# Kernel tuning notes

Hardware: AMD Instinct MI355X
Metric: run time of the kernel (lower is better)

Reference implementation:

```python
import jax, jax.numpy as jnp
import numpy as np

INPUT_SIZE = 64
HIDDEN = 128
BATCH = 512
SEQ = 512


def setup_inputs() -> dict:
    key = jax.random.key(0)
    ks = jax.random.split(key, 7)
    s_ih = 1.0 / np.sqrt(HIDDEN)
    token = jax.random.normal(ks[0], (BATCH, SEQ, INPUT_SIZE), dtype=jnp.float32)
    W_ih = jax.random.uniform(ks[1], (HIDDEN, INPUT_SIZE), jnp.float32, -s_ih, s_ih)
    W_hh = jax.random.uniform(ks[2], (HIDDEN, HIDDEN), jnp.float32, -s_ih, s_ih)
    b_ih = jax.random.uniform(ks[3], (HIDDEN,), jnp.float32, -s_ih, s_ih)
    b_hh = jax.random.uniform(ks[4], (HIDDEN,), jnp.float32, -s_ih, s_ih)
    W_lin = jax.random.uniform(ks[5], (1, HIDDEN), jnp.float32, -s_ih, s_ih)
    b_lin = jax.random.uniform(ks[6], (1,), jnp.float32, -s_ih, s_ih)
    return {"token": token, "W_ih": W_ih, "W_hh": W_hh, "b_ih": b_ih,
            "b_hh": b_hh, "W_lin": W_lin, "b_lin": b_lin}


def reference(token, W_ih, W_hh, b_ih, b_hh, W_lin, b_lin):
    # Precompute input projection for all timesteps: [T, B, H]
    x_proj = jnp.einsum('bti,hi->tbh', token, W_ih) + b_ih + b_hh
    h0 = jnp.zeros((token.shape[0], W_hh.shape[0]), dtype=token.dtype)

    def step(h, xp):
        h_new = jnp.tanh(xp + h @ W_hh.T)
        return h_new, None

    h_last, _ = jax.lax.scan(step, h0, x_proj)
    # Linear head on last hidden state: [B, 1]
    return h_last @ W_lin.T + b_lin
```

## Files before the change

### kernel.cpp

```cpp
#include <hip/hip_runtime.h>

#define B_ 512
#define T_ 512
#define I_ 64
#define H_ 128

#define HB0    0
#define HB1    512
#define DUMMY  1024
#define LDS_SZ 1280

#define FM(a, x, w) "v_fmac_f32 v" #a ", v" #x ", v" #w "\n\t"
#define SC(n) "v_mul_f32 v" #n ", 0x4038aa3b, v" #n "\n\t"

#define CLOBS \
    "v48","v49","v50","v51","v52","v53","v54","v55","v56","v57","v58","v59", \
    "v60","v61","v62","v63","v64","v65","v66","v67","v68","v69","v70","v71", \
    "v72","v73","v74","v75","v76","v77","v78","v79","v80","v81","v82","v83", \
    "v84","v85","v86","v87","v88","v89","v90","v91","v92","v93","v94","v95", \
    "v96","v97","v98","v99","v100","v101","v102","v103","v104","v105","v106", \
    "v107","v108","v109","v110","v111","v112","v113","v114","v115","v116", \
    "v117","v118","v119","v120","v121","v122","v123","v124","v125","v126", \
    "v127","memory"

#define RNN_STEP(TA, TB, TC, TD, HRD, HWR)                                    \
    asm volatile(                                                             \
        "ds_read_b128 v[72:75], %1\n\t"                                       \
        "ds_read_b128 v[76:79], %1 offset:256\n\t"                            \
        "s_waitcnt vmcnt(3)\n\t"                                              \
        "v_fma_f32 v48, v" #TA ", v112, %3\n\t"                               \
        "v_fma_f32 v49, v" #TA ", v116, %4\n\t"                               \
        "v_fma_f32 v50, v" #TA ", v120, %5\n\t"                               \
        "v_fma_f32 v51, v" #TA ", v124, %6\n\t"                               \
        FM(48,TB,113) FM(49,TB,117) FM(50,TB,121) FM(51,TB,125)               \
        FM(48,TC,114) FM(49,TC,118) FM(50,TC,122) FM(51,TC,126)               \
        FM(48,TD,115) FM(49,TD,119) FM(50,TD,123) FM(51,TD,127)               \
        "global_load_dwordx4 v[" #TA ":" #TD "], %0, %9\n\t"                  \
        "v_add_u32 %0, 0x100, %0\n\t"                                         \
        "v_and_b32 %0, 0x1ffff, %0\n\t"                                       \
        "s_waitcnt lgkmcnt(1)\n\t"                                            \
        FM(48,72,80) FM(49,72,88) FM(50,72,96)  FM(51,72,104)                 \
        FM(48,73,81) FM(49,73,89) FM(50,73,97)  FM(51,73,105)                 \
        FM(48,74,82) FM(49,74,90) FM(50,74,98)  FM(51,74,106)                 \
        FM(48,75,83) FM(49,75,91) FM(50,75,99)  FM(51,75,107)                 \
        "s_waitcnt lgkmcnt(0)\n\t"                                            \
        FM(48,76,84) FM(49,76,92) FM(50,76,100) FM(51,76,108)                 \
        FM(48,77,85) FM(49,77,93) FM(50,77,101) FM(51,77,109)                 \
        FM(48,78,86) FM(49,78,94) FM(50,78,102) FM(51,78,110)                 \
        FM(48,79,87) FM(49,79,95) FM(50,79,103) FM(51,79,111)                 \
        "s_nop 1\n\t"                                                         \
        "v_add_f32 v48, v48, v48 quad_perm:[1,0,3,2] row_mask:0xf bank_mask:0xf\n\t" \
        "v_add_f32 v49, v49, v49 quad_perm:[1,0,3,2] row_mask:0xf bank_mask:0xf\n\t" \
        "v_add_f32 v50, v50, v50 quad_perm:[1,0,3,2] row_mask:0xf bank_mask:0xf\n\t" \
        "v_add_f32 v51, v51, v51 quad_perm:[1,0,3,2] row_mask:0xf bank_mask:0xf\n\t" \
        "v_cndmask_b32 v52, v48, v49, %7\n\t"                                 \
        "v_cndmask_b32 v53, v50, v51, %7\n\t"                                 \
        "s_nop 0\n\t"                                                         \
        "v_add_f32 v52, v52, v52 quad_perm:[2,3,0,1] row_mask:0xf bank_mask:0xf\n\t" \
        "v_add_f32 v53, v53, v53 quad_perm:[2,3,0,1] row_mask:0xf bank_mask:0xf\n\t" \
        "v_cndmask_b32 v54, v52, v53, %8\n\t"                                 \
        "s_nop 1\n\t"                                                         \
        "v_add_f32 v54, v54, v54 row_shl:8 row_mask:0xf bank_mask:0x3\n\t"    \
        "s_nop 1\n\t"                                                         \
        "v_add_f32 v54, v54, v54 row_shl:4 row_mask:0xf bank_mask:0x1\n\t"    \
        "s_nop 1\n\t"                                                         \
        "v_exp_f32 v54, v54\n\t"                                              \
        "s_nop 0\n\t"                                                         \
        "v_add_f32 v54, 1.0, v54\n\t"                                         \
        "v_rcp_f32 v55, v54\n\t"                                              \
        "s_nop 0\n\t"                                                         \
        "v_fma_f32 v54, v55, -2.0, 1.0\n\t"                                   \
        "ds_write_b32 %2, v54\n\t"                                            \
        "s_waitcnt lgkmcnt(0)\n\t"                                            \
        "s_barrier"                                                           \
        : "+v"(voff)                                                          \
        : "v"(HRD), "v"(HWR), "v"(biasA), "v"(biasB), "v"(biasC),             \
          "v"(biasD), "s"(M1), "s"(M2), "s"(sbase)                            \
        : CLOBS)

__global__ __launch_bounds__(512) __attribute__((amdgpu_waves_per_eu(4, 4)))
void rnn_kernel(const float* __restrict__ token,
                const float* __restrict__ W_ih,
                const float* __restrict__ W_hh,
                const float* __restrict__ b_ih,
                const float* __restrict__ b_hh,
                const float* __restrict__ W_lin,
                const float* __restrict__ b_lin,
                float* __restrict__ out)
{
    __shared__ __align__(16) char lds[LDS_SZ];
    const unsigned lb =
        (unsigned)(uintptr_t)(__attribute__((address_space(3))) char*)lds;

    const int tid = threadIdx.x;
    const int e   = tid & 15;
    const int G   = tid >> 4;
    const int b   = blockIdx.x;
    const int jb  = 4 * G;

    {
        const float* pWh = W_hh + jb * H_ + e * 8;
        const float* pWi = W_ih + jb * I_ + e * 4;
        asm volatile(
            "global_load_dwordx4 v[80:83],   %0, off\n\t"
            "global_load_dwordx4 v[84:87],   %0, off offset:16\n\t"
            "global_load_dwordx4 v[88:91],   %0, off offset:512\n\t"
            "global_load_dwordx4 v[92:95],   %0, off offset:528\n\t"
            "global_load_dwordx4 v[96:99],   %0, off offset:1024\n\t"
            "global_load_dwordx4 v[100:103], %0, off offset:1040\n\t"
            "global_load_dwordx4 v[104:107], %0, off offset:1536\n\t"
            "global_load_dwordx4 v[108:111], %0, off offset:1552\n\t"
            "global_load_dwordx4 v[112:115], %1, off\n\t"
            "global_load_dwordx4 v[116:119], %1, off offset:256\n\t"
            "global_load_dwordx4 v[120:123], %1, off offset:512\n\t"
            "global_load_dwordx4 v[124:127], %1, off offset:768\n\t"
            "s_waitcnt vmcnt(0)\n\t"
            SC(80) SC(81) SC(82) SC(83) SC(84) SC(85) SC(86) SC(87)
            SC(88) SC(89) SC(90) SC(91) SC(92) SC(93) SC(94) SC(95)
            SC(96) SC(97) SC(98) SC(99) SC(100) SC(101) SC(102) SC(103)
            SC(104) SC(105) SC(106) SC(107) SC(108) SC(109) SC(110) SC(111)
            SC(112) SC(113) SC(114) SC(115) SC(116) SC(117) SC(118) SC(119)
            SC(120) SC(121) SC(122) SC(123) SC(124) SC(125) SC(126) SC(127)
            :: "v"(pWh), "v"(pWi) : CLOBS);
    }

    const float k16 = 2.885390081777927f / 16.0f;
    const float biasA = (b_ih[jb + 0] + b_hh[jb + 0]) * k16;
    const float biasB = (b_ih[jb + 1] + b_hh[jb + 1]) * k16;
    const float biasC = (b_ih[jb + 2] + b_hh[jb + 2]) * k16;
    const float biasD = (b_ih[jb + 3] + b_hh[jb + 3]) * k16;
    const unsigned long long M1 = 0xAAAAAAAAAAAAAAAAULL;
    const unsigned long long M2 = 0xCCCCCCCCCCCCCCCCULL;

    const int  jsel   = jb + (e & 3);
    const int  wbyte  = ((((jsel >> 2) & 1) * 16 + (jsel >> 3)) * 16) + (jsel & 3) * 4;
    const bool writer = (e < 4);
    const unsigned dmy = lb + DUMMY + (tid & 63) * 4;
    const unsigned hw0 = writer ? (lb + HB1 + wbyte) : dmy;
    const unsigned hw1 = writer ? (lb + HB0 + wbyte) : dmy;
    const unsigned hr0 = lb + HB0 + e * 16;
    const unsigned hr1 = lb + HB1 + e * 16;

    const float* tok_row = token + (size_t)b * T_ * I_;
    const unsigned long long sbase = (unsigned long long)(uintptr_t)tok_row;

    {
        const unsigned v0 = e * 16;
        asm volatile(
            "global_load_dwordx4 v[56:59], %0, %1\n\t"
            "global_load_dwordx4 v[60:63], %0, %1 offset:256\n\t"
            "global_load_dwordx4 v[64:67], %0, %1 offset:512\n\t"
            "global_load_dwordx4 v[68:71], %0, %1 offset:768\n\t"
            :: "v"(v0), "s"(sbase) : CLOBS);
    }
    unsigned voff = e * 16 + 1024;
    if (tid < H_) *(float*)(lds + HB0 + tid * 4) = 0.0f;
    asm volatile("s_waitcnt lgkmcnt(0)\n\ts_barrier" ::: "memory");

#pragma unroll 1
    for (int t = 0; t < T_; t += 4) {
        RNN_STEP(56, 57, 58, 59, hr0, hw0);
        RNN_STEP(60, 61, 62, 63, hr1, hw1);
        RNN_STEP(64, 65, 66, 67, hr0, hw0);
        RNN_STEP(68, 69, 70, 71, hr1, hw1);
    }

    asm volatile("s_waitcnt vmcnt(0)" ::: "memory");

    if (tid < 64) {
        const int a0 = tid, a1 = tid + 64;
        const int l0 = (((a0 >> 2) & 1) * 16 + (a0 >> 3)) * 4 + (a0 & 3);
        const int l1 = (((a1 >> 2) & 1) * 16 + (a1 >> 3)) * 4 + (a1 & 3);
        float p = *(const float*)(lds + HB0 + l0 * 4) * W_lin[a0]
                + *(const float*)(lds + HB0 + l1 * 4) * W_lin[a1];
#pragma unroll
        for (int off = 32; off; off >>= 1) p += __shfl_down(p, off);
        if (tid == 0) out[b] = p + b_lin[0];
    }
}

extern "C" void kernel_launch(void* const* d_in, const int* in_sizes, int n_in,
                              void* d_out, int out_size, void* d_ws, size_t ws_size,
                              hipStream_t stream) {
    const float* token = (const float*)d_in[0];
    const float* W_ih  = (const float*)d_in[1];
    const float* W_hh  = (const float*)d_in[2];
    const float* b_ih  = (const float*)d_in[3];
    const float* b_hh  = (const float*)d_in[4];
    const float* W_lin = (const float*)d_in[5];
    const float* b_lin = (const float*)d_in[6];
    float* out = (float*)d_out;

    hipLaunchKernelGGL(rnn_kernel, dim3(B_), dim3(512), 0, stream,
                       token, W_ih, W_hh, b_ih, b_hh, W_lin, b_lin, out);
}
```

Measured before the change: 197.9 us.

## Store hidden state and W_hh in bf16, use v_dot2 for recurrence

Converts the recurrent weights to packed bf16 in registers and stores the hidden state in LDS as bf16. Each step then needs one ds_read_b128 instead of two and 16 v_dot2_f32_bf16 instead of 32 FMAs on the serial critical path. The LDS layout changes to a plain contiguous bf16 vector, and the output head decodes bf16. This trades accuracy: the hidden state is rounded to bf16 on every one of 512 steps, so error can accumulate.

```diff
diff --git a/kernel.cpp b/kernel.cpp
--- a/kernel.cpp
+++ b/kernel.cpp
@@ -6,9 +6,9 @@
 #define H_ 128
 
 #define HB0    0
-#define HB1    512
-#define DUMMY  1024
-#define LDS_SZ 1280
+#define HB1    256
+#define DUMMY  512
+#define LDS_SZ 1536
 
 #define FM(a, x, w) "v_fmac_f32 v" #a ", v" #x ", v" #w "\n\t"
 #define SC(n) "v_mul_f32 v" #n ", 0x4038aa3b, v" #n "\n\t"
@@ -26,7 +26,6 @@
 #define RNN_STEP(TA, TB, TC, TD, HRD, HWR)                                    \
     asm volatile(                                                             \
         "ds_read_b128 v[72:75], %1\n\t"                                       \
-        "ds_read_b128 v[76:79], %1 offset:256\n\t"                            \
         "s_waitcnt vmcnt(3)\n\t"                                              \
         "v_fma_f32 v48, v" #TA ", v112, %3\n\t"                               \
         "v_fma_f32 v49, v" #TA ", v116, %4\n\t"                               \
@@ -38,16 +37,23 @@
         "global_load_dwordx4 v[" #TA ":" #TD "], %0, %9\n\t"                  \
         "v_add_u32 %0, 0x100, %0\n\t"                                         \
         "v_and_b32 %0, 0x1ffff, %0\n\t"                                       \
-        "s_waitcnt lgkmcnt(1)\n\t"                                            \
-        FM(48,72,80) FM(49,72,88) FM(50,72,96)  FM(51,72,104)                 \
-        FM(48,73,81) FM(49,73,89) FM(50,73,97)  FM(51,73,105)                 \
-        FM(48,74,82) FM(49,74,90) FM(50,74,98)  FM(51,74,106)                 \
-        FM(48,75,83) FM(49,75,91) FM(50,75,99)  FM(51,75,107)                 \
         "s_waitcnt lgkmcnt(0)\n\t"                                            \
-        FM(48,76,84) FM(49,76,92) FM(50,76,100) FM(51,76,108)                 \
-        FM(48,77,85) FM(49,77,93) FM(50,77,101) FM(51,77,109)                 \
-        FM(48,78,86) FM(49,78,94) FM(50,78,102) FM(51,78,110)                 \
-        FM(48,79,87) FM(49,79,95) FM(50,79,103) FM(51,79,111)                 \
+        "v_dot2_f32_bf16 v48, v72, v80, v48\n\t"                              \
+        "v_dot2_f32_bf16 v49, v72, v84, v49\n\t"                              \
+        "v_dot2_f32_bf16 v50, v72, v88, v50\n\t"                              \
+        "v_dot2_f32_bf16 v51, v72, v92, v51\n\t"                              \
+        "v_dot2_f32_bf16 v48, v73, v81, v48\n\t"                              \
+        "v_dot2_f32_bf16 v49, v73, v85, v49\n\t"                              \
+        "v_dot2_f32_bf16 v50, v73, v89, v50\n\t"                              \
+        "v_dot2_f32_bf16 v51, v73, v93, v51\n\t"                              \
+        "v_dot2_f32_bf16 v48, v74, v82, v48\n\t"                              \
+        "v_dot2_f32_bf16 v49, v74, v86, v49\n\t"                              \
+        "v_dot2_f32_bf16 v50, v74, v90, v50\n\t"                              \
+        "v_dot2_f32_bf16 v51, v74, v94, v51\n\t"                              \
+        "v_dot2_f32_bf16 v48, v75, v83, v48\n\t"                              \
+        "v_dot2_f32_bf16 v49, v75, v87, v49\n\t"                              \
+        "v_dot2_f32_bf16 v50, v75, v91, v50\n\t"                              \
+        "v_dot2_f32_bf16 v51, v75, v95, v51\n\t"                              \
         "s_nop 1\n\t"                                                         \
         "v_add_f32 v48, v48, v48 quad_perm:[1,0,3,2] row_mask:0xf bank_mask:0xf\n\t" \
         "v_add_f32 v49, v49, v49 quad_perm:[1,0,3,2] row_mask:0xf bank_mask:0xf\n\t" \
@@ -70,7 +76,8 @@
         "v_rcp_f32 v55, v54\n\t"                                              \
         "s_nop 0\n\t"                                                         \
         "v_fma_f32 v54, v55, -2.0, 1.0\n\t"                                   \
-        "ds_write_b32 %2, v54\n\t"                                            \
+        "v_cvt_pk_bf16_f32 v54, v54, v54\n\t"                                 \
+        "ds_write_b16 %2, v54\n\t"                                            \
         "s_waitcnt lgkmcnt(0)\n\t"                                            \
         "s_barrier"                                                           \
         : "+v"(voff)                                                          \
@@ -100,28 +107,49 @@
 
     {
         const float* pWh = W_hh + jb * H_ + e * 8;
+        asm volatile(
+            "global_load_dwordx4 v[48:51], %0, off\n\t"
+            "global_load_dwordx4 v[52:55], %0, off offset:16\n\t"
+            "global_load_dwordx4 v[56:59], %0, off offset:512\n\t"
+            "global_load_dwordx4 v[60:63], %0, off offset:528\n\t"
+            "global_load_dwordx4 v[64:67], %0, off offset:1024\n\t"
+            "global_load_dwordx4 v[68:71], %0, off offset:1040\n\t"
+            "global_load_dwordx4 v[72:75], %0, off offset:1536\n\t"
+            "global_load_dwordx4 v[76:79], %0, off offset:1552\n\t"
+            "s_waitcnt vmcnt(0)\n\t"
+            SC(48) SC(49) SC(50) SC(51) SC(52) SC(53) SC(54) SC(55)
+            SC(56) SC(57) SC(58) SC(59) SC(60) SC(61) SC(62) SC(63)
+            SC(64) SC(65) SC(66) SC(67) SC(68) SC(69) SC(70) SC(71)
+            SC(72) SC(73) SC(74) SC(75) SC(76) SC(77) SC(78) SC(79)
+            "v_cvt_pk_bf16_f32 v80, v48, v49\n\t"
+            "v_cvt_pk_bf16_f32 v81, v50, v51\n\t"
+            "v_cvt_pk_bf16_f32 v82, v52, v53\n\t"
+            "v_cvt_pk_bf16_f32 v83, v54, v55\n\t"
+            "v_cvt_pk_bf16_f32 v84, v56, v57\n\t"
+            "v_cvt_pk_bf16_f32 v85, v58, v59\n\t"
+            "v_cvt_pk_bf16_f32 v86, v60, v61\n\t"
+            "v_cvt_pk_bf16_f32 v87, v62, v63\n\t"
+            "v_cvt_pk_bf16_f32 v88, v64, v65\n\t"
+            "v_cvt_pk_bf16_f32 v89, v66, v67\n\t"
+            "v_cvt_pk_bf16_f32 v90, v68, v69\n\t"
+            "v_cvt_pk_bf16_f32 v91, v70, v71\n\t"
+            "v_cvt_pk_bf16_f32 v92, v72, v73\n\t"
+            "v_cvt_pk_bf16_f32 v93, v74, v75\n\t"
+            "v_cvt_pk_bf16_f32 v94, v76, v77\n\t"
+            "v_cvt_pk_bf16_f32 v95, v78, v79\n\t"
+            :: "v"(pWh) : CLOBS);
+    }
+    {
         const float* pWi = W_ih + jb * I_ + e * 4;
         asm volatile(
-            "global_load_dwordx4 v[80:83],   %0, off\n\t"
-            "global_load_dwordx4 v[84:87],   %0, off offset:16\n\t"
-            "global_load_dwordx4 v[88:91],   %0, off offset:512\n\t"
-            "global_load_dwordx4 v[92:95],   %0, off offset:528\n\t"
-            "global_load_dwordx4 v[96:99],   %0, off offset:1024\n\t"
-            "global_load_dwordx4 v[100:103], %0, off offset:1040\n\t"
-            "global_load_dwordx4 v[104:107], %0, off offset:1536\n\t"
-            "global_load_dwordx4 v[108:111], %0, off offset:1552\n\t"
-            "global_load_dwordx4 v[112:115], %1, off\n\t"
-            "global_load_dwordx4 v[116:119], %1, off offset:256\n\t"
-            "global_load_dwordx4 v[120:123], %1, off offset:512\n\t"
-            "global_load_dwordx4 v[124:127], %1, off offset:768\n\t"
+            "global_load_dwordx4 v[112:115], %0, off\n\t"
+            "global_load_dwordx4 v[116:119], %0, off offset:256\n\t"
+            "global_load_dwordx4 v[120:123], %0, off offset:512\n\t"
+            "global_load_dwordx4 v[124:127], %0, off offset:768\n\t"
             "s_waitcnt vmcnt(0)\n\t"
-            SC(80) SC(81) SC(82) SC(83) SC(84) SC(85) SC(86) SC(87)
-            SC(88) SC(89) SC(90) SC(91) SC(92) SC(93) SC(94) SC(95)
-            SC(96) SC(97) SC(98) SC(99) SC(100) SC(101) SC(102) SC(103)
-            SC(104) SC(105) SC(106) SC(107) SC(108) SC(109) SC(110) SC(111)
             SC(112) SC(113) SC(114) SC(115) SC(116) SC(117) SC(118) SC(119)
             SC(120) SC(121) SC(122) SC(123) SC(124) SC(125) SC(126) SC(127)
-            :: "v"(pWh), "v"(pWi) : CLOBS);
+            :: "v"(pWi) : CLOBS);
     }
 
     const float k16 = 2.885390081777927f / 16.0f;
@@ -133,11 +161,10 @@
     const unsigned long long M2 = 0xCCCCCCCCCCCCCCCCULL;
 
     const int  jsel   = jb + (e & 3);
-    const int  wbyte  = ((((jsel >> 2) & 1) * 16 + (jsel >> 3)) * 16) + (jsel & 3) * 4;
     const bool writer = (e < 4);
-    const unsigned dmy = lb + DUMMY + (tid & 63) * 4;
-    const unsigned hw0 = writer ? (lb + HB1 + wbyte) : dmy;
-    const unsigned hw1 = writer ? (lb + HB0 + wbyte) : dmy;
+    const unsigned dmy = lb + DUMMY + tid * 2;
+    const unsigned hw0 = writer ? (lb + HB1 + jsel * 2) : dmy;
+    const unsigned hw1 = writer ? (lb + HB0 + jsel * 2) : dmy;
     const unsigned hr0 = lb + HB0 + e * 16;
     const unsigned hr1 = lb + HB1 + e * 16;
 
@@ -154,7 +181,7 @@
             :: "v"(v0), "s"(sbase) : CLOBS);
     }
     unsigned voff = e * 16 + 1024;
-    if (tid < H_) *(float*)(lds + HB0 + tid * 4) = 0.0f;
+    if (tid < H_) *(unsigned short*)(lds + HB0 + tid * 2) = 0;
     asm volatile("s_waitcnt lgkmcnt(0)\n\ts_barrier" ::: "memory");
 
 #pragma unroll 1
@@ -168,11 +195,11 @@
     asm volatile("s_waitcnt vmcnt(0)" ::: "memory");
 
     if (tid < 64) {
-        const int a0 = tid, a1 = tid + 64;
-        const int l0 = (((a0 >> 2) & 1) * 16 + (a0 >> 3)) * 4 + (a0 & 3);
-        const int l1 = (((a1 >> 2) & 1) * 16 + (a1 >> 3)) * 4 + (a1 & 3);
-        float p = *(const float*)(lds + HB0 + l0 * 4) * W_lin[a0]
-                + *(const float*)(lds + HB0 + l1 * 4) * W_lin[a1];
+        unsigned u0 = *(const unsigned short*)(lds + HB0 + 2 * tid);
+        unsigned u1 = *(const unsigned short*)(lds + HB0 + 2 * (tid + 64));
+        float h0 = __uint_as_float(u0 << 16);
+        float h1 = __uint_as_float(u1 << 16);
+        float p = h0 * W_lin[tid] + h1 * W_lin[tid + 64];
 #pragma unroll
         for (int off = 32; off; off >>= 1) p += __shfl_down(p, off);
         if (tid == 0) out[b] = p + b_lin[0];
```

New measurement: 208.4 us. +5.3%, slower.

## Process two batch rows per block with interleaved recurrences sharing one barrier

Applied to the files above, without the earlier changes.

Each workgroup now runs two independent batch rows, interleaving their RNN steps so one row's math can overlap the other's LDS round trip, and issues only one barrier per pair of steps. The grid is halved to B/2 blocks and separate LDS ping-pong buffers and token prefetch registers are added for the second row. This trades doubled serial work per block and fewer blocks (256 versus 512 on a 256-CU part) for amortised barrier and latency costs in the serial recurrence.

```diff
diff --git a/kernel.cpp b/kernel.cpp
--- a/kernel.cpp
+++ b/kernel.cpp
@@ -5,29 +5,32 @@
 #define I_ 64
 #define H_ 128
 
-#define HB0    0
-#define HB1    512
-#define DUMMY  1024
-#define LDS_SZ 1280
+#define HA0    0
+#define HA1    512
+#define HBB0   1024
+#define HBB1   1536
+#define DUMMY  2048
+#define LDS_SZ 2304
 
 #define FM(a, x, w) "v_fmac_f32 v" #a ", v" #x ", v" #w "\n\t"
 #define SC(n) "v_mul_f32 v" #n ", 0x4038aa3b, v" #n "\n\t"
 
 #define CLOBS \
-    "v48","v49","v50","v51","v52","v53","v54","v55","v56","v57","v58","v59", \
-    "v60","v61","v62","v63","v64","v65","v66","v67","v68","v69","v70","v71", \
-    "v72","v73","v74","v75","v76","v77","v78","v79","v80","v81","v82","v83", \
-    "v84","v85","v86","v87","v88","v89","v90","v91","v92","v93","v94","v95", \
-    "v96","v97","v98","v99","v100","v101","v102","v103","v104","v105","v106", \
-    "v107","v108","v109","v110","v111","v112","v113","v114","v115","v116", \
-    "v117","v118","v119","v120","v121","v122","v123","v124","v125","v126", \
-    "v127","memory"
-
-#define RNN_STEP(TA, TB, TC, TD, HRD, HWR)                                    \
+    "v32","v33","v34","v35","v36","v37","v38","v39","v40","v41","v42","v43", \
+    "v44","v45","v46","v47","v48","v49","v50","v51","v52","v53","v54","v55", \
+    "v56","v57","v58","v59","v60","v61","v62","v63","v64","v65","v66","v67", \
+    "v68","v69","v70","v71","v72","v73","v74","v75","v76","v77","v78","v79", \
+    "v80","v81","v82","v83","v84","v85","v86","v87","v88","v89","v90","v91", \
+    "v92","v93","v94","v95","v96","v97","v98","v99","v100","v101","v102", \
+    "v103","v104","v105","v106","v107","v108","v109","v110","v111","v112", \
+    "v113","v114","v115","v116","v117","v118","v119","v120","v121","v122", \
+    "v123","v124","v125","v126","v127","memory"
+
+#define RNN_STEP(TA, TB, TC, TD, VOFF, HRD, HWR, SB, TAIL)                    \
     asm volatile(                                                             \
         "ds_read_b128 v[72:75], %1\n\t"                                       \
         "ds_read_b128 v[76:79], %1 offset:256\n\t"                            \
-        "s_waitcnt vmcnt(3)\n\t"                                              \
+        "s_waitcnt vmcnt(7)\n\t"                                              \
         "v_fma_f32 v48, v" #TA ", v112, %3\n\t"                               \
         "v_fma_f32 v49, v" #TA ", v116, %4\n\t"                               \
         "v_fma_f32 v50, v" #TA ", v120, %5\n\t"                               \
@@ -71,12 +74,14 @@
         "s_nop 0\n\t"                                                         \
         "v_fma_f32 v54, v55, -2.0, 1.0\n\t"                                   \
         "ds_write_b32 %2, v54\n\t"                                            \
-        "s_waitcnt lgkmcnt(0)\n\t"                                            \
-        "s_barrier"                                                           \
-        : "+v"(voff)                                                          \
+        TAIL                                                                  \
+        : "+v"(VOFF)                                                          \
         : "v"(HRD), "v"(HWR), "v"(biasA), "v"(biasB), "v"(biasC),             \
-          "v"(biasD), "s"(M1), "s"(M2), "s"(sbase)                            \
+          "v"(biasD), "s"(M1), "s"(M2), "s"(SB)                               \
         : CLOBS)
+
+#define TAIL_A ""
+#define TAIL_B "s_waitcnt lgkmcnt(0)\n\ts_barrier"
 
 __global__ __launch_bounds__(512) __attribute__((amdgpu_waves_per_eu(4, 4)))
 void rnn_kernel(const float* __restrict__ token,
@@ -135,47 +140,67 @@
     const int  jsel   = jb + (e & 3);
     const int  wbyte  = ((((jsel >> 2) & 1) * 16 + (jsel >> 3)) * 16) + (jsel & 3) * 4;
     const bool writer = (e < 4);
-    const unsigned dmy = lb + DUMMY + (tid & 63) * 4;
-    const unsigned hw0 = writer ? (lb + HB1 + wbyte) : dmy;
-    const unsigned hw1 = writer ? (lb + HB0 + wbyte) : dmy;
-    const unsigned hr0 = lb + HB0 + e * 16;
-    const unsigned hr1 = lb + HB1 + e * 16;
-
-    const float* tok_row = token + (size_t)b * T_ * I_;
-    const unsigned long long sbase = (unsigned long long)(uintptr_t)tok_row;
+    const unsigned dmy  = lb + DUMMY + (tid & 63) * 4;
+    const unsigned hwA0 = writer ? (lb + HA1 + wbyte) : dmy;
+    const unsigned hwA1 = writer ? (lb + HA0 + wbyte) : dmy;
+    const unsigned hwB0 = writer ? (lb + HBB1 + wbyte) : dmy;
+    const unsigned hwB1 = writer ? (lb + HBB0 + wbyte) : dmy;
+    const unsigned hrA0 = lb + HA0 + e * 16;
+    const unsigned hrA1 = lb + HA1 + e * 16;
+    const unsigned hrB0 = lb + HBB0 + e * 16;
+    const unsigned hrB1 = lb + HBB1 + e * 16;
+
+    const unsigned long long sbA =
+        (unsigned long long)(uintptr_t)(token + (size_t)(2 * b) * T_ * I_);
+    const unsigned long long sbB =
+        (unsigned long long)(uintptr_t)(token + (size_t)(2 * b + 1) * T_ * I_);
 
     {
         const unsigned v0 = e * 16;
         asm volatile(
             "global_load_dwordx4 v[56:59], %0, %1\n\t"
+            "global_load_dwordx4 v[32:35], %0, %2\n\t"
             "global_load_dwordx4 v[60:63], %0, %1 offset:256\n\t"
+            "global_load_dwordx4 v[36:39], %0, %2 offset:256\n\t"
             "global_load_dwordx4 v[64:67], %0, %1 offset:512\n\t"
+            "global_load_dwordx4 v[40:43], %0, %2 offset:512\n\t"
             "global_load_dwordx4 v[68:71], %0, %1 offset:768\n\t"
-            :: "v"(v0), "s"(sbase) : CLOBS);
-    }
-    unsigned voff = e * 16 + 1024;
-    if (tid < H_) *(float*)(lds + HB0 + tid * 4) = 0.0f;
+            "global_load_dwordx4 v[44:47], %0, %2 offset:768\n\t"
+            :: "v"(v0), "s"(sbA), "s"(sbB) : CLOBS);
+    }
+    unsigned voffA = e * 16 + 1024;
+    unsigned voffB = e * 16 + 1024;
+    if (tid < H_) {
+        *(float*)(lds + HA0  + tid * 4) = 0.0f;
+        *(float*)(lds + HBB0 + tid * 4) = 0.0f;
+    }
     asm volatile("s_waitcnt lgkmcnt(0)\n\ts_barrier" ::: "memory");
 
 #pragma unroll 1
     for (int t = 0; t < T_; t += 4) {
-        RNN_STEP(56, 57, 58, 59, hr0, hw0);
-        RNN_STEP(60, 61, 62, 63, hr1, hw1);
-        RNN_STEP(64, 65, 66, 67, hr0, hw0);
-        RNN_STEP(68, 69, 70, 71, hr1, hw1);
+        RNN_STEP(56, 57, 58, 59, voffA, hrA0, hwA0, sbA, TAIL_A);
+        RNN_STEP(32, 33, 34, 35, voffB, hrB0, hwB0, sbB, TAIL_B);
+        RNN_STEP(60, 61, 62, 63, voffA, hrA1, hwA1, sbA, TAIL_A);
+        RNN_STEP(36, 37, 38, 39, voffB, hrB1, hwB1, sbB, TAIL_B);
+        RNN_STEP(64, 65, 66, 67, voffA, hrA0, hwA0, sbA, TAIL_A);
+        RNN_STEP(40, 41, 42, 43, voffB, hrB0, hwB0, sbB, TAIL_B);
+        RNN_STEP(68, 69, 70, 71, voffA, hrA1, hwA1, sbA, TAIL_A);
+        RNN_STEP(44, 45, 46, 47, voffB, hrB1, hwB1, sbB, TAIL_B);
     }
 
     asm volatile("s_waitcnt vmcnt(0)" ::: "memory");
 
-    if (tid < 64) {
-        const int a0 = tid, a1 = tid + 64;
-        const int l0 = (((a0 >> 2) & 1) * 16 + (a0 >> 3)) * 4 + (a0 & 3);
-        const int l1 = (((a1 >> 2) & 1) * 16 + (a1 >> 3)) * 4 + (a1 & 3);
-        float p = *(const float*)(lds + HB0 + l0 * 4) * W_lin[a0]
-                + *(const float*)(lds + HB0 + l1 * 4) * W_lin[a1];
+    if (tid < 128) {
+        const int row = tid >> 6;
+        const int a0  = tid & 63, a1 = (tid & 63) + 64;
+        const int l0  = (((a0 >> 2) & 1) * 16 + (a0 >> 3)) * 4 + (a0 & 3);
+        const int l1  = (((a1 >> 2) & 1) * 16 + (a1 >> 3)) * 4 + (a1 & 3);
+        const int hb  = row ? HBB0 : HA0;
+        float p = *(const float*)(lds + hb + l0 * 4) * W_lin[a0]
+                + *(const float*)(lds + hb + l1 * 4) * W_lin[a1];
 #pragma unroll
         for (int off = 32; off; off >>= 1) p += __shfl_down(p, off);
-        if (tid == 0) out[b] = p + b_lin[0];
+        if ((tid & 63) == 0) out[2 * b + row] = p + b_lin[0];
     }
 }
 
@@ -191,6 +216,6 @@
     const float* b_lin = (const float*)d_in[6];
     float* out = (float*)d_out;
 
-    hipLaunchKernelGGL(rnn_kernel, dim3(B_), dim3(512), 0, stream,
+    hipLaunchKernelGGL(rnn_kernel, dim3(B_ / 2), dim3(512), 0, stream,
                        token, W_ih, W_hh, b_ih, b_hh, W_lin, b_lin, out);
 }
```

Result: slower. 241.4 us (+22.0%).
